# Optimization experiments

Hardware: AMD Instinct MI355X
Metric: run time of the kernel (lower is better)

## Reference

```python
import jax, jax.numpy as jnp
import numpy as np

B, N_HEADS, F_TOK = 8, 12, 768
GRID_H, GRID_W = 32, 32
N_TOK = 1 + GRID_H * GRID_W  # 1025 (readout token + patches)
F_HEAD = F_TOK // N_HEADS    # 64
NUM_DIST = (2 * GRID_H - 1) * (2 * GRID_W - 1) + 3  # 3972


def _build_relpos_index(gh, gw):
    # BEiT-style relative position index with 3 extra slots for the readout token
    coords = np.stack(np.meshgrid(np.arange(gh), np.arange(gw), indexing='ij'))  # (2, gh, gw)
    flat = coords.reshape(2, -1)                                                 # (2, gh*gw)
    rel = flat[:, :, None] - flat[:, None, :]                                    # (2, P, P)
    rel = rel.transpose(1, 2, 0).astype(np.int64)                                # (P, P, 2)
    rel[:, :, 0] += gh - 1
    rel[:, :, 1] += gw - 1
    rel[:, :, 0] *= 2 * gw - 1
    rpi = rel.sum(-1)                                                            # (P, P)
    n = 1 + gh * gw
    nd = (2 * gh - 1) * (2 * gw - 1) + 3
    idx = np.zeros((n, n), dtype=np.int32)
    idx[1:, 1:] = rpi
    idx[0, :] = nd - 3  # readout -> all
    idx[:, 0] = nd - 2  # all -> readout
    idx[0, 0] = nd - 1  # readout -> readout
    return idx


def setup_inputs() -> dict:
    key = jax.random.key(0)
    ks = jax.random.split(key, 7)
    tokens = jax.random.normal(ks[0], (B, N_TOK, F_TOK), dtype=jnp.float32)
    qkv_w = jax.random.normal(ks[1], (3 * F_TOK, F_TOK), dtype=jnp.float32) * 0.02
    q_bias = jax.random.normal(ks[2], (1, N_HEADS, 1, F_HEAD), dtype=jnp.float32) * 0.02
    v_bias = jax.random.normal(ks[3], (1, N_HEADS, 1, F_HEAD), dtype=jnp.float32) * 0.02
    relpos_table = jax.random.normal(ks[4], (NUM_DIST, N_HEADS), dtype=jnp.float32) * 0.02
    proj_w = jax.random.normal(ks[5], (F_TOK, F_TOK), dtype=jnp.float32) * 0.02
    proj_b = jax.random.normal(ks[6], (F_TOK,), dtype=jnp.float32) * 0.02
    relpos_index = jnp.asarray(_build_relpos_index(GRID_H, GRID_W))  # (N, N) int32
    return {
        'tokens': tokens, 'qkv_w': qkv_w, 'q_bias': q_bias, 'v_bias': v_bias,
        'relpos_table': relpos_table, 'proj_w': proj_w, 'proj_b': proj_b,
        'relpos_index': relpos_index, 'patch_h': GRID_H, 'patch_w': GRID_W,
    }


def reference(tokens, qkv_w, q_bias, v_bias, relpos_table, proj_w, proj_b,
              relpos_index, patch_h, patch_w):
    b, n, f_tok = tokens.shape
    # qkv projection (no bias): (B, N, 3F) -> (3, B, H, N, f)
    qkv = tokens @ qkv_w.T
    qkv = qkv.reshape(b, n, 3, N_HEADS, F_HEAD).transpose(2, 0, 3, 1, 4)
    q, k, v = qkv[0], qkv[1], qkv[2]
    q = (q + q_bias) * (F_HEAD ** -0.5)
    v = v + v_bias
    # attention scores: (B, H, N, N)
    attn = jnp.einsum('bhnf,bhmf->bhnm', q, k)
    # relative position bias gather: (N, N, H) -> (H, N, N)
    bias = relpos_table[relpos_index].transpose(2, 0, 1)
    attn = attn + bias[None]
    w = jax.nn.softmax(attn, axis=-1)
    out = jnp.einsum('bhnm,bhmf->bhnf', w, v)
    out = out.transpose(0, 2, 1, 3).reshape(b, n, N_HEADS * F_HEAD)
    return out @ proj_w.T + proj_b
```

## Files before the change

kernel.cpp:

```cpp
#include <hip/hip_runtime.h>

#define B_ 8
#define NH 12
#define NTOK 1025
#define FT 768
#define MROWS (B_*NTOK)
#define NPAD2 1088
#define CH 17
#define NQT 36
#define NTT 34
#define NRT18 18

typedef __bf16 bf16x8 __attribute__((ext_vector_type(8)));
typedef __bf16 bf16x2 __attribute__((ext_vector_type(2)));
typedef float floatx4 __attribute__((ext_vector_type(4)));
typedef float floatx16 __attribute__((ext_vector_type(16)));
typedef int intx4 __attribute__((ext_vector_type(4)));

__device__ __forceinline__ void async_ld16(const void* gp, void* lp) {
  __builtin_amdgcn_global_load_lds(
      (const __attribute__((address_space(1))) void*)gp,
      (__attribute__((address_space(3))) void*)lp, 16, 0, 0);
}

__global__ __launch_bounds__(256) void cvt_bf16(const float* __restrict__ src,
                                                __bf16* __restrict__ dst, int n4) {
  int i = blockIdx.x * 256 + threadIdx.x;
  if (i >= n4) return;
  float4 v = ((const float4*)src)[i];
  __bf16 o[4] = {(__bf16)v.x, (__bf16)v.y, (__bf16)v.z, (__bf16)v.w};
  *(uint2*)(dst + 4 * (size_t)i) = *(uint2*)o;
}

__global__ __launch_bounds__(256) void bias_gather_t(
    const int* __restrict__ idx, const float* __restrict__ table,
    __bf16* __restrict__ Bb) {
  const int qt = blockIdx.x, tt = blockIdx.y;
  const int t = threadIdx.x;
  const int lane = t & 63, w = t >> 6;
  const int l31 = lane & 31, hb = lane >> 5;
  int qrow = qt * 32 + l31; if (qrow > NTOK - 1) qrow = NTOK - 1;
  int ids[16]; bool ok[16];
#pragma unroll
  for (int j = 0; j < 16; ++j) {
    const int token = tt * 32 + (j & 3) + 8 * (j >> 2) + 4 * hb;
    ok[j] = token < NTOK;
    ids[j] = ok[j] ? idx[qrow * NTOK + token] : 0;
  }
#pragma unroll
  for (int g = 0; g < 3; ++g) {
    const int h = w + g * 4;
    __bf16 v[16];
#pragma unroll
    for (int j = 0; j < 16; ++j)
      v[j] = ok[j] ? (__bf16)table[ids[j] * NH + h] : (__bf16)(-1e30f);
    uint4* dst = (uint4*)(Bb + (((size_t)h * NQT + qt) * NTT + tt) * 1024 + lane * 16);
    dst[0] = ((uint4*)v)[0];
    dst[1] = ((uint4*)v)[1];
  }
}

__device__ __forceinline__ void gemm128_pipe(
    const __bf16* __restrict__ A, const __bf16* __restrict__ W,
    int m0, int n0, int M, __bf16* At, __bf16* Bt, floatx4 acc[4][4]) {
  const int tid = threadIdx.x, wave = tid >> 6, lane = tid & 63;
  const int l = lane & 15, qd = lane >> 4;
  const int wr = wave >> 1, wc = wave & 1;
  const int srow = lane >> 2, sg = lane & 3;
  const int r0 = wave * 32 + srow, r1 = r0 + 16;
  int gm0 = m0 + r0; if (gm0 >= M) gm0 = M - 1;
  int gm1 = m0 + r1; if (gm1 >= M) gm1 = M - 1;
  const int sw0 = (sg ^ (r0 & 3)) * 8;
  const __bf16* gA0 = A + (size_t)gm0 * FT + sw0;
  const __bf16* gA1 = A + (size_t)gm1 * FT + sw0;
  const __bf16* gB0 = W + (size_t)(n0 + r0) * FT + sw0;
  const __bf16* gB1 = W + (size_t)(n0 + r1) * FT + sw0;
  const int woff = wave * 32 * 32;
  const int fsw = (qd ^ (l & 3)) * 8;

  auto issue = [&](int k, int buf) {
    __bf16* a = At + buf * 4096 + woff;
    __bf16* b = Bt + buf * 4096 + woff;
    async_ld16(gA0 + k * 32, a);
    async_ld16(gA1 + k * 32, a + 512);
    async_ld16(gB0 + k * 32, b);
    async_ld16(gB1 + k * 32, b + 512);
  };
  auto step = [&](int buf) {
    __builtin_amdgcn_s_barrier();
    const __bf16* ab = At + buf * 4096;
    const __bf16* bb = Bt + buf * 4096;
    bf16x8 aF[4], bF[4];
#pragma unroll
    for (int t = 0; t < 4; ++t)
      aF[t] = *(const bf16x8*)(ab + (wr * 64 + t * 16 + l) * 32 + fsw);
#pragma unroll
    for (int u = 0; u < 4; ++u)
      bF[u] = *(const bf16x8*)(bb + (wc * 64 + u * 16 + l) * 32 + fsw);
#pragma unroll
    for (int t = 0; t < 4; ++t)
#pragma unroll
      for (int u = 0; u < 4; ++u)
        acc[t][u] = __builtin_amdgcn_mfma_f32_16x16x32_bf16(aF[t], bF[u], acc[t][u], 0, 0, 0);
  };

  issue(0, 0);
  int bk = 0;
  for (int k = 0; k < 23; ++k) {
    int bn = bk + 1; if (bn == 3) bn = 0;
    issue(k + 1, bn);
    __builtin_amdgcn_s_waitcnt(0x0F74);
    step(bk);
    bk = bn;
  }
  __builtin_amdgcn_s_waitcnt(0x0F70);
  step(bk);
}

__global__ __launch_bounds__(256) void qkv_gemm128(
    const __bf16* __restrict__ tokens, const __bf16* __restrict__ qkvw,
    const float* __restrict__ qbias, const float* __restrict__ vbias,
    __bf16* __restrict__ Qb, __bf16* __restrict__ Kc, __bf16* __restrict__ Vc) {
  __shared__ __bf16 At[3 * 4096], Bt[3 * 4096];
  const int u0 = blockIdx.x;
  const int c = u0 & 7, q0 = u0 >> 3;
  const int mi = (q0 / 18) * 8 + c, ni = q0 % 18;
  if (mi >= 65) return;
  const int m0 = mi * 128, n0 = ni * 128;
  const int tid = threadIdx.x, wave = tid >> 6, lane = tid & 63;
  const int l = lane & 15, qd = lane >> 4;
  const int wr = wave >> 1, wc = wave & 1;
  floatx4 acc[4][4];
#pragma unroll
  for (int t = 0; t < 4; ++t)
#pragma unroll
    for (int u = 0; u < 4; ++u) acc[t][u] = (floatx4){0.f, 0.f, 0.f, 0.f};
  gemm128_pipe(tokens, qkvw, m0, n0, MROWS, At, Bt, acc);

  const int which = (n0 / FT);
  const int nrem0 = n0 - which * FT;
#pragma unroll
  for (int u = 0; u < 4; ++u) {
    const int rem = nrem0 + wc * 64 + u * 16 + l;
    const int h = rem >> 6, f = rem & 63;
    const float qb = (which == 0) ? qbias[h * 64 + f] : 0.f;
    const float vb = (which == 2) ? vbias[h * 64 + f] : 0.f;
#pragma unroll
    for (int t = 0; t < 4; ++t) {
#pragma unroll
      for (int r = 0; r < 4; ++r) {
        const int gm = m0 + wr * 64 + t * 16 + qd * 4 + r;
        if (gm >= MROWS) continue;
        const int b = gm / NTOK;
        const int tok = gm - b * NTOK;
        const size_t bh = (size_t)(b * NH + h);
        float v = acc[t][u][r];
        if (which == 0) {
          Qb[(bh * NPAD2 + tok) * 64 + f] = (__bf16)((v + qb) * 0.125f);
        } else if (which == 1) {
          const size_t e = ((size_t)(bh * CH + (tok >> 6))) * 4096 +
                           (((f >> 3) * 64 + (tok & 63)) << 3) + (f & 7);
          Kc[e] = (__bf16)v;
        } else {
          const size_t e = ((size_t)(bh * CH + (tok >> 6))) * 4096 +
                           (((((tok >> 3) & 7) * 64 + f)) << 3) + (tok & 7);
          Vc[e] = (__bf16)(v + vb);
        }
      }
    }
  }
}

__global__ __launch_bounds__(256) void proj_gemm128(
    const __bf16* __restrict__ Ao, const __bf16* __restrict__ projw,
    const float* __restrict__ projb, float* __restrict__ out) {
  __shared__ __bf16 At[3 * 4096], Bt[3 * 4096];
  const int u0 = blockIdx.x;
  const int c = u0 & 7, q0 = u0 >> 3;
  const int mi = (q0 / 6) * 8 + c, ni = q0 % 6;
  if (mi >= 65) return;
  const int m0 = mi * 128, n0 = ni * 128;
  const int tid = threadIdx.x, wave = tid >> 6, lane = tid & 63;
  const int l = lane & 15, qd = lane >> 4;
  const int wr = wave >> 1, wc = wave & 1;
  floatx4 acc[4][4];
#pragma unroll
  for (int t = 0; t < 4; ++t)
#pragma unroll
    for (int u = 0; u < 4; ++u) acc[t][u] = (floatx4){0.f, 0.f, 0.f, 0.f};
  gemm128_pipe(Ao, projw, m0, n0, MROWS, At, Bt, acc);
#pragma unroll
  for (int u = 0; u < 4; ++u) {
    const int gn = n0 + wc * 64 + u * 16 + l;
    const float pb = projb[gn];
#pragma unroll
    for (int t = 0; t < 4; ++t)
#pragma unroll
      for (int r = 0; r < 4; ++r) {
        const int gm = m0 + wr * 64 + t * 16 + qd * 4 + r;
        if (gm < MROWS) out[(size_t)gm * FT + gn] = acc[t][u][r] + pb;
      }
  }
}

__global__ __launch_bounds__(128) void attn_flash(
    const __bf16* __restrict__ Qb, const __bf16* __restrict__ Kc,
    const __bf16* __restrict__ Vc, const __bf16* __restrict__ Bb,
    __bf16* __restrict__ Ao) {
  __shared__ __bf16 Kl[4096], Vl[4096];
  const int bh = blockIdx.x;
  const int rt = blockIdx.y;
  const int h = bh % NH, b = bh / NH;
  const int wave = threadIdx.x >> 6, lane = threadIdx.x & 63;
  const int l31 = lane & 31, hb = lane >> 5;
  const int qt = rt * 2 + wave;
  int qrow = qt * 32 + l31; if (qrow > NTOK - 1) qrow = NTOK - 1;

  bf16x8 qf[4];
  {
    const __bf16* Qp = Qb + ((size_t)bh * NPAD2 + qrow) * 64 + hb * 8;
#pragma unroll
    for (int d = 0; d < 4; ++d) qf[d] = *(const bf16x8*)(Qp + d * 16);
  }

  floatx16 o0, o1;
#pragma unroll
  for (int j = 0; j < 16; ++j) { o0[j] = 0.f; o1[j] = 0.f; }
  float lsum = 0.f;

  const __bf16* Kg = Kc + (size_t)bh * CH * 4096;
  const __bf16* Vg = Vc + (size_t)bh * CH * 4096;
  const __bf16* Bg = Bb + ((size_t)h * NQT + qt) * NTT * 1024 + lane * 16;

  for (int c = 0; c < CH; ++c) {
    {
      const __bf16* gk = Kg + c * 4096;
      const __bf16* gv = Vg + c * 4096;
#pragma unroll
      for (int ii = 0; ii < 8; ++ii) {
        const int i = wave * 8 + ii;
        const __bf16* src = (i < 8) ? (gk + i * 512) : (gv + (i - 8) * 512);
        __bf16* dst = (i < 8) ? (Kl + i * 512) : (Vl + (i - 8) * 512);
        async_ld16(src + lane * 8, dst);
      }
    }
    __syncthreads();

    int pk[2][8];
#pragma unroll
    for (int tt = 0; tt < 2; ++tt) {
      floatx16 st;
#pragma unroll
      for (int j = 0; j < 16; ++j) st[j] = 0.f;
#pragma unroll
      for (int dk = 0; dk < 4; ++dk) {
        bf16x8 a = *(const bf16x8*)(Kl + (((dk * 2 + hb) * 64) + tt * 32 + l31) * 8);
        st = __builtin_amdgcn_mfma_f32_32x32x16_bf16(a, qf[dk], st, 0, 0, 0);
      }
      bf16x8 b0 = *(const bf16x8*)(Bg + (size_t)(c * 2 + tt) * 1024);
      bf16x8 b1 = *(const bf16x8*)(Bg + (size_t)(c * 2 + tt) * 1024 + 8);
      float e[16];
#pragma unroll
      for (int j = 0; j < 16; ++j) {
        const float bj = (float)(j < 8 ? b0[j] : b1[j - 8]);
        e[j] = __expf(st[j] + bj);
        lsum += e[j];
      }
#pragma unroll
      for (int j2 = 0; j2 < 8; ++j2) {
        bf16x2 pr = {(__bf16)e[2 * j2], (__bf16)e[2 * j2 + 1]};
        pk[tt][j2] = __builtin_bit_cast(int, pr);
      }
    }

#pragma unroll
    for (int ks = 0; ks < 4; ++ks) {
      const int s = ks & 1, tt = ks >> 1;
      const int r01a = pk[tt][4 * s + 0], r01b = pk[tt][4 * s + 1];
      const int r23a = pk[tt][4 * s + 2], r23b = pk[tt][4 * s + 3];
      const int t01a = __shfl_xor(r01a, 32), t01b = __shfl_xor(r01b, 32);
      const int t23a = __shfl_xor(r23a, 32), t23b = __shfl_xor(r23b, 32);
      intx4 fi;
      fi[0] = hb ? t23a : r01a;
      fi[1] = hb ? t23b : r01b;
      fi[2] = hb ? r23a : t01a;
      fi[3] = hb ? r23b : t01b;
      bf16x8 pb = __builtin_bit_cast(bf16x8, fi);
      bf16x8 va0 = *(const bf16x8*)(Vl + (((ks * 2 + hb) * 64) + l31) * 8);
      bf16x8 va1 = *(const bf16x8*)(Vl + (((ks * 2 + hb) * 64) + 32 + l31) * 8);
      o0 = __builtin_amdgcn_mfma_f32_32x32x16_bf16(va0, pb, o0, 0, 0, 0);
      o1 = __builtin_amdgcn_mfma_f32_32x32x16_bf16(va1, pb, o1, 0, 0, 0);
    }
    __syncthreads();
  }

  const float ltot = lsum + __shfl_xor(lsum, 32);
  const float rinv = 1.0f / ltot;
  const int tok = rt * 64 + wave * 32 + l31;
  if (tok < NTOK) {
    __bf16* op = Ao + ((size_t)b * NTOK + tok) * FT + h * 64;
#pragma unroll
    for (int ft = 0; ft < 2; ++ft) {
#pragma unroll
      for (int jg = 0; jg < 4; ++jg) {
        const int f = ft * 32 + jg * 8 + hb * 4;
        __bf16 v4[4];
#pragma unroll
        for (int q = 0; q < 4; ++q) {
          const float ov = ft ? o1[jg * 4 + q] : o0[jg * 4 + q];
          v4[q] = (__bf16)(ov * rinv);
        }
        *(uint2*)(op + f) = *(uint2*)v4;
      }
    }
  }
}

extern "C" void kernel_launch(void* const* d_in, const int* in_sizes, int n_in,
                              void* d_out, int out_size, void* d_ws, size_t ws_size,
                              hipStream_t stream) {
  (void)in_sizes; (void)n_in; (void)out_size; (void)ws_size;
  const float* tokens = (const float*)d_in[0];
  const float* qkvw   = (const float*)d_in[1];
  const float* qbias  = (const float*)d_in[2];
  const float* vbias  = (const float*)d_in[3];
  const float* table  = (const float*)d_in[4];
  const float* projw  = (const float*)d_in[5];
  const float* projb  = (const float*)d_in[6];
  const int*   rpidx  = (const int*)d_in[7];
  float* out = (float*)d_out;
  char* ws = (char*)d_ws;

  const size_t QB2 = (size_t)B_ * NH * NPAD2 * 64 * 2;
  const size_t BBT = (size_t)NH * NQT * NTT * 1024 * 2;
  const size_t AOB = (size_t)MROWS * FT * 2;
  const size_t WQB = (size_t)3 * FT * FT * 2;
  __bf16* Qb = (__bf16*)(ws);
  __bf16* Kc = (__bf16*)(ws + QB2);
  __bf16* Vc = (__bf16*)(ws + 2 * QB2);
  __bf16* Bb = (__bf16*)(ws + 3 * QB2);
  __bf16* Tb = (__bf16*)(ws + 3 * QB2 + BBT);
  __bf16* Ao = Tb;
  __bf16* Wq = (__bf16*)(ws + 3 * QB2 + BBT + AOB);
  __bf16* Wp = (__bf16*)(ws + 3 * QB2 + BBT + AOB + WQB);

  cvt_bf16<<<(MROWS * FT / 4 + 255) / 256, 256, 0, stream>>>(tokens, Tb, MROWS * FT / 4);
  cvt_bf16<<<(3 * FT * FT / 4 + 255) / 256, 256, 0, stream>>>(qkvw, Wq, 3 * FT * FT / 4);
  cvt_bf16<<<(FT * FT / 4 + 255) / 256, 256, 0, stream>>>(projw, Wp, FT * FT / 4);
  bias_gather_t<<<dim3(NQT, NTT), 256, 0, stream>>>(rpidx, table, Bb);
  qkv_gemm128<<<8 * 9 * 18, 256, 0, stream>>>(Tb, Wq, qbias, vbias, Qb, Kc, Vc);
  attn_flash<<<dim3(B_ * NH, NRT18), 128, 0, stream>>>(Qb, Kc, Vc, Bb, Ao);
  proj_gemm128<<<8 * 9 * 6, 256, 0, stream>>>(Ao, Wp, projb, out);
}
```

Measured before the change: 275.7 us.

## Triple-buffer K/V chunks in attention with async prefetch and exp2 softmax

Splits the K/V chunks into 32-token pieces and changes the layout the QKV GEMM epilogue writes to match. The attention loop now prefetches the next chunk into a three-slot shared-memory ring, with one wave loading K and the other V, and uses a single barrier per iteration. The aim is to overlap global loads with MFMA and exp work instead of stalling at two syncthreads per chunk. Log2(e) is folded into the Q scale and the bias table so the softmax can use hardware exp2. The trade-off is twice as many loop iterations and more shared memory, and correctness depends on hand-encoded waitcnt values.

```diff
diff --git a/kernel.cpp b/kernel.cpp
--- a/kernel.cpp
+++ b/kernel.cpp
@@ -6,10 +6,11 @@
 #define FT 768
 #define MROWS (B_*NTOK)
 #define NPAD2 1088
-#define CH 17
+#define CH2 34
 #define NQT 36
 #define NTT 34
 #define NRT18 18
+#define LOG2E 1.44269504089f
 
 typedef __bf16 bf16x8 __attribute__((ext_vector_type(8)));
 typedef __bf16 bf16x2 __attribute__((ext_vector_type(2)));
@@ -53,7 +54,7 @@
     __bf16 v[16];
 #pragma unroll
     for (int j = 0; j < 16; ++j)
-      v[j] = ok[j] ? (__bf16)table[ids[j] * NH + h] : (__bf16)(-1e30f);
+      v[j] = ok[j] ? (__bf16)(table[ids[j] * NH + h] * LOG2E) : (__bf16)(-1e30f);
     uint4* dst = (uint4*)(Bb + (((size_t)h * NQT + qt) * NTT + tt) * 1024 + lane * 16);
     dst[0] = ((uint4*)v)[0];
     dst[1] = ((uint4*)v)[1];
@@ -156,14 +157,14 @@
         const size_t bh = (size_t)(b * NH + h);
         float v = acc[t][u][r];
         if (which == 0) {
-          Qb[(bh * NPAD2 + tok) * 64 + f] = (__bf16)((v + qb) * 0.125f);
+          Qb[(bh * NPAD2 + tok) * 64 + f] = (__bf16)((v + qb) * (0.125f * LOG2E));
         } else if (which == 1) {
-          const size_t e = ((size_t)(bh * CH + (tok >> 6))) * 4096 +
-                           (((f >> 3) * 64 + (tok & 63)) << 3) + (f & 7);
+          const size_t e = ((size_t)(bh * CH2 + (tok >> 5))) * 2048 +
+                           (((f >> 3) * 32 + (tok & 31)) << 3) + (f & 7);
           Kc[e] = (__bf16)v;
         } else {
-          const size_t e = ((size_t)(bh * CH + (tok >> 6))) * 4096 +
-                           (((((tok >> 3) & 7) * 64 + f)) << 3) + (tok & 7);
+          const size_t e = ((size_t)(bh * CH2 + (tok >> 5))) * 2048 +
+                           (((((tok >> 3) & 3) * 64 + f)) << 3) + (tok & 7);
           Vc[e] = (__bf16)(v + vb);
         }
       }
@@ -207,7 +208,7 @@
     const __bf16* __restrict__ Qb, const __bf16* __restrict__ Kc,
     const __bf16* __restrict__ Vc, const __bf16* __restrict__ Bb,
     __bf16* __restrict__ Ao) {
-  __shared__ __bf16 Kl[4096], Vl[4096];
+  __shared__ __bf16 Kl[3][2048], Vl[3][2048];
   const int bh = blockIdx.x;
   const int rt = blockIdx.y;
   const int h = bh % NH, b = bh / NH;
@@ -228,56 +229,58 @@
   for (int j = 0; j < 16; ++j) { o0[j] = 0.f; o1[j] = 0.f; }
   float lsum = 0.f;
 
-  const __bf16* Kg = Kc + (size_t)bh * CH * 4096;
-  const __bf16* Vg = Vc + (size_t)bh * CH * 4096;
+  const __bf16* KVg = (wave ? Vc : Kc) + (size_t)bh * CH2 * 2048;
   const __bf16* Bg = Bb + ((size_t)h * NQT + qt) * NTT * 1024 + lane * 16;
 
-  for (int c = 0; c < CH; ++c) {
-    {
-      const __bf16* gk = Kg + c * 4096;
-      const __bf16* gv = Vg + c * 4096;
-#pragma unroll
-      for (int ii = 0; ii < 8; ++ii) {
-        const int i = wave * 8 + ii;
-        const __bf16* src = (i < 8) ? (gk + i * 512) : (gv + (i - 8) * 512);
-        __bf16* dst = (i < 8) ? (Kl + i * 512) : (Vl + (i - 8) * 512);
-        async_ld16(src + lane * 8, dst);
-      }
-    }
-    __syncthreads();
-
-    int pk[2][8];
-#pragma unroll
-    for (int tt = 0; tt < 2; ++tt) {
-      floatx16 st;
-#pragma unroll
-      for (int j = 0; j < 16; ++j) st[j] = 0.f;
-#pragma unroll
-      for (int dk = 0; dk < 4; ++dk) {
-        bf16x8 a = *(const bf16x8*)(Kl + (((dk * 2 + hb) * 64) + tt * 32 + l31) * 8);
-        st = __builtin_amdgcn_mfma_f32_32x32x16_bf16(a, qf[dk], st, 0, 0, 0);
-      }
-      bf16x8 b0 = *(const bf16x8*)(Bg + (size_t)(c * 2 + tt) * 1024);
-      bf16x8 b1 = *(const bf16x8*)(Bg + (size_t)(c * 2 + tt) * 1024 + 8);
-      float e[16];
-#pragma unroll
-      for (int j = 0; j < 16; ++j) {
-        const float bj = (float)(j < 8 ? b0[j] : b1[j - 8]);
-        e[j] = __expf(st[j] + bj);
-        lsum += e[j];
-      }
-#pragma unroll
-      for (int j2 = 0; j2 < 8; ++j2) {
-        bf16x2 pr = {(__bf16)e[2 * j2], (__bf16)e[2 * j2 + 1]};
-        pk[tt][j2] = __builtin_bit_cast(int, pr);
-      }
-    }
-
-#pragma unroll
-    for (int ks = 0; ks < 4; ++ks) {
-      const int s = ks & 1, tt = ks >> 1;
-      const int r01a = pk[tt][4 * s + 0], r01b = pk[tt][4 * s + 1];
-      const int r23a = pk[tt][4 * s + 2], r23b = pk[tt][4 * s + 3];
+  auto issue = [&](int c, int buf) {
+    const __bf16* src = KVg + (size_t)c * 2048 + lane * 8;
+    __bf16* dst = wave ? Vl[buf] : Kl[buf];
+#pragma unroll
+    for (int ii = 0; ii < 4; ++ii) async_ld16(src + ii * 512, dst + ii * 512);
+  };
+
+  issue(0, 0);
+  bf16x8 bc0 = *(const bf16x8*)(Bg);
+  bf16x8 bc1 = *(const bf16x8*)(Bg + 8);
+  int buf = 0;
+  for (int c = 0; c < CH2; ++c) {
+    int nbuf = buf + 1; if (nbuf == 3) nbuf = 0;
+    bf16x8 bn0 = bc0, bn1 = bc1;
+    if (c + 1 < CH2) {
+      issue(c + 1, nbuf);
+      bn0 = *(const bf16x8*)(Bg + (size_t)(c + 1) * 1024);
+      bn1 = *(const bf16x8*)(Bg + (size_t)(c + 1) * 1024 + 8);
+      __builtin_amdgcn_s_waitcnt(0x0F76);
+    } else {
+      __builtin_amdgcn_s_waitcnt(0x0F70);
+    }
+    __builtin_amdgcn_s_barrier();
+
+    floatx16 st;
+#pragma unroll
+    for (int j = 0; j < 16; ++j) st[j] = 0.f;
+#pragma unroll
+    for (int dk = 0; dk < 4; ++dk) {
+      bf16x8 a = *(const bf16x8*)(Kl[buf] + ((dk * 2 + hb) * 32 + l31) * 8);
+      st = __builtin_amdgcn_mfma_f32_32x32x16_bf16(a, qf[dk], st, 0, 0, 0);
+    }
+    float e[16];
+#pragma unroll
+    for (int j = 0; j < 16; ++j) {
+      const float bj = (float)(j < 8 ? bc0[j] : bc1[j - 8]);
+      e[j] = __builtin_amdgcn_exp2f(st[j] + bj);
+      lsum += e[j];
+    }
+    int pk[8];
+#pragma unroll
+    for (int j2 = 0; j2 < 8; ++j2) {
+      bf16x2 pr = {(__bf16)e[2 * j2], (__bf16)e[2 * j2 + 1]};
+      pk[j2] = __builtin_bit_cast(int, pr);
+    }
+#pragma unroll
+    for (int ks = 0; ks < 2; ++ks) {
+      const int r01a = pk[4 * ks + 0], r01b = pk[4 * ks + 1];
+      const int r23a = pk[4 * ks + 2], r23b = pk[4 * ks + 3];
       const int t01a = __shfl_xor(r01a, 32), t01b = __shfl_xor(r01b, 32);
       const int t23a = __shfl_xor(r23a, 32), t23b = __shfl_xor(r23b, 32);
       intx4 fi;
@@ -286,12 +289,13 @@
       fi[2] = hb ? r23a : t01a;
       fi[3] = hb ? r23b : t01b;
       bf16x8 pb = __builtin_bit_cast(bf16x8, fi);
-      bf16x8 va0 = *(const bf16x8*)(Vl + (((ks * 2 + hb) * 64) + l31) * 8);
-      bf16x8 va1 = *(const bf16x8*)(Vl + (((ks * 2 + hb) * 64) + 32 + l31) * 8);
+      bf16x8 va0 = *(const bf16x8*)(Vl[buf] + ((ks * 2 + hb) * 64 + l31) * 8);
+      bf16x8 va1 = *(const bf16x8*)(Vl[buf] + ((ks * 2 + hb) * 64 + 32 + l31) * 8);
       o0 = __builtin_amdgcn_mfma_f32_32x32x16_bf16(va0, pb, o0, 0, 0, 0);
       o1 = __builtin_amdgcn_mfma_f32_32x32x16_bf16(va1, pb, o1, 0, 0, 0);
     }
-    __syncthreads();
+    bc0 = bn0; bc1 = bn1;
+    buf = nbuf;
   }
 
   const float ltot = lsum + __shfl_xor(lsum, 32);
```

Result: no change. 273.1 us (-0.9%).
